# Optimization experiments

Hardware: AMD Instinct MI355X
Metric: run time of the kernel (lower is better)

The kernel has to match this reference:

```python
import jax, jax.numpy as jnp
import numpy as np

B, N, P, K = 4, 512, 1024, 20
LMAX, SH_DIM, MUL, NB = 2, 9, 64, 20
CUT, T, NSPEC = 4.0, 3, 119
E = N * K
PE = P * K
L_SLICES = [(0, 1), (1, 4), (4, 9)]


def spherical_harmonics(vec):
    # component-normalized real SH up to l=2 on the unit vector (e3nn 'component' norm: ||Y_l||^2 = 2l+1)
    r = jnp.sqrt(jnp.sum(vec * vec, axis=-1, keepdims=True))
    u = vec / jnp.maximum(r, 1e-9)
    x, y, z = u[:, 0], u[:, 1], u[:, 2]
    s3, s5, s15 = 3.0 ** 0.5, 5.0 ** 0.5, 15.0 ** 0.5
    return jnp.stack([
        jnp.ones_like(x),
        s3 * x, s3 * y, s3 * z,
        s15 * x * y, s15 * y * z, 0.5 * s5 * (3.0 * z * z - 1.0),
        s15 * x * z, 0.5 * s15 * (x * x - y * y),
    ], axis=-1)  # [E, 9]


def radial_basis(r):
    # gaussian RBF, centers linspace(0, cutoff, num_basis)
    centers = jnp.linspace(0.0, CUT, NB)
    sigma = CUT / NB
    return jnp.exp(-((r[:, None] - centers[None, :]) / sigma) ** 2)


def per_l_linear(a, Wl):
    # a: [n, 9, mul]; Wl: [3, mul, mul]; independent channel-mixing per angular momentum l
    return jnp.concatenate([a[:, s:e, :] @ Wl[l] for l, (s, e) in enumerate(L_SLICES)], axis=1)


def conv_layer(h_src_feats, sh, rbf, src, dst, n_out, Wr1, br1, Wr2, br2, Wl, Wg):
    # radial MLP -> per-edge weights; gather scalar source features; tensor-product-style message sh (x) (w*s)
    w = jax.nn.silu(rbf @ Wr1 + br1) @ Wr2 + br2                 # [E, mul]
    s_src = h_src_feats[src, 0, :]                               # [E, mul]
    m = sh[:, :, None] * (s_src * w)[:, None, :]                 # [E, 9, mul]
    a = jax.ops.segment_sum(m, dst, num_segments=n_out) / (K ** 0.5)
    u = per_l_linear(a, Wl)                                      # [n, 9, mul]
    gate = jax.nn.sigmoid(a[:, 0, :] @ Wg)                       # gate activation for l>0
    return jnp.concatenate([jax.nn.silu(u[:, :1, :]), u[:, 1:, :] * gate[:, None, :]], axis=1)


def _forward(atom_xyz, atom_edges_displacement, cell, probe_xyz, probe_edges_displacement,
             W_embed, Wr1, br1, Wr2, br2, Wl, Wg,
             pWr1, pbr1, pWr2, pbr2, pWl, pWg, W_out,
             atom_edges, probe_edges, nodes):
    Na, Np, Et, PEt = B * N, B * P, B * E, B * PE
    pos = atom_xyz.reshape(Na, 3)          # unpad_and_cat with uniform lengths == reshape
    ppos = probe_xyz.reshape(Np, 3)
    node_off = (jnp.arange(B, dtype=atom_edges.dtype) * N)[:, None, None]
    a_edges = (atom_edges + node_off).reshape(Et, 2)
    p_off = jnp.concatenate([node_off, (jnp.arange(B, dtype=atom_edges.dtype) * P)[:, None, None]], axis=2)
    p_edges = (probe_edges + p_off).reshape(PEt, 2)
    # fractional displacement -> cartesian via per-graph cell (repeat_interleave over edges)
    cell_a = jnp.repeat(cell, E, axis=0)
    cell_p = jnp.repeat(cell, PE, axis=0)
    disp_a = jnp.einsum('ei,eij->ej', atom_edges_displacement.reshape(Et, 3), cell_a)
    disp_p = jnp.einsum('ei,eij->ej', probe_edges_displacement.reshape(PEt, 3), cell_p)
    src, dst = a_edges[:, 0], a_edges[:, 1]
    edge_vec = pos[dst] - (pos[src] + disp_a)
    sh = spherical_harmonics(edge_vec)
    rbf = radial_basis(jnp.linalg.norm(edge_vec, axis=1))
    psrc, pdst = p_edges[:, 0], p_edges[:, 1]
    p_vec = ppos[pdst] - (pos[psrc] + disp_p)
    psh = spherical_harmonics(p_vec)
    prbf = radial_basis(jnp.linalg.norm(p_vec, axis=1))
    # AtomicConfigurationModel: one-hot species -> scalar channel, T interaction layers, keep per-layer reps
    onehot = jax.nn.one_hot(nodes.reshape(Na), NSPEC, dtype=W_embed.dtype)
    h = jnp.zeros((Na, SH_DIM, MUL), W_embed.dtype).at[:, 0, :].set(onehot @ W_embed)
    reps = []
    for t in range(T):
        h = h + conv_layer(h, sh, rbf, src, dst, Na, Wr1[t], br1[t], Wr2[t], br2[t], Wl[t], Wg[t])
        reps.append(h)
    # AtomicPotentialModel: atom->probe message passing using per-layer atom representations
    p = jnp.zeros((Np, SH_DIM, MUL), W_embed.dtype)
    for t in range(T):
        p = p + conv_layer(reps[t], psh, prbf, psrc, pdst, Np, pWr1[t], pbr1[t], pWr2[t], pbr2[t], pWl[t], pWg[t])
    out = (p[:, 0, :] @ W_out)[:, 0].reshape(B, P)  # readout to 0e scalar, pad_and_stack == reshape
    return out


def setup_inputs():
    key = jax.random.key(0)
    ks = jax.random.split(key, 20)
    f32 = jnp.float32
    atom_xyz = jax.random.uniform(ks[0], (B, N, 3), f32) * 8.0
    probe_xyz = jax.random.uniform(ks[1], (B, P, 3), f32) * 8.0
    cell = jnp.tile(jnp.eye(3, dtype=f32)[None] * 8.0, (B, 1, 1))
    atom_edges = jax.random.randint(ks[2], (B, E, 2), 0, N, jnp.int32)
    probe_edges = jnp.concatenate([
        jax.random.randint(ks[3], (B, PE, 1), 0, N, jnp.int32),
        jax.random.randint(ks[4], (B, PE, 1), 0, P, jnp.int32)], axis=2)
    atom_edges_displacement = jax.random.randint(ks[5], (B, E, 3), -1, 2).astype(f32)
    probe_edges_displacement = jax.random.randint(ks[6], (B, PE, 3), -1, 2).astype(f32)
    nodes = jax.random.randint(ks[7], (B, N), 1, 84, jnp.int32)
    num_nodes = jnp.full((B,), N, jnp.int32)
    num_atom_edges = jnp.full((B,), E, jnp.int32)
    num_probes = jnp.full((B,), P, jnp.int32)
    num_probe_edges = jnp.full((B,), PE, jnp.int32)
    rn = lambda k, s: jax.random.normal(k, s, f32) * 0.1
    W_embed = rn(ks[8], (NSPEC, MUL))
    Wr1 = rn(ks[9], (T, NB, 100)); br1 = jnp.zeros((T, 100), f32)
    Wr2 = rn(ks[10], (T, 100, MUL)); br2 = jnp.zeros((T, MUL), f32)
    Wl = rn(ks[11], (T, 3, MUL, MUL)); Wg = rn(ks[12], (T, MUL, MUL))
    pWr1 = rn(ks[13], (T, NB, 100)); pbr1 = jnp.zeros((T, 100), f32)
    pWr2 = rn(ks[14], (T, 100, MUL)); pbr2 = jnp.zeros((T, MUL), f32)
    pWl = rn(ks[15], (T, 3, MUL, MUL)); pWg = rn(ks[16], (T, MUL, MUL))
    W_out = rn(ks[17], (MUL, 1))
    return dict(atom_xyz=atom_xyz, atom_edges_displacement=atom_edges_displacement, cell=cell,
                probe_xyz=probe_xyz, probe_edges_displacement=probe_edges_displacement,
                W_embed=W_embed, Wr1=Wr1, br1=br1, Wr2=Wr2, br2=br2, Wl=Wl, Wg=Wg,
                pWr1=pWr1, pbr1=pbr1, pWr2=pWr2, pbr2=pbr2, pWl=pWl, pWg=pWg, W_out=W_out,
                atom_edges=atom_edges, probe_edges=probe_edges, nodes=nodes,
                num_nodes=num_nodes, num_atom_edges=num_atom_edges,
                num_probes=num_probes, num_probe_edges=num_probe_edges)


def reference(atom_xyz, atom_edges_displacement, cell, probe_xyz, probe_edges_displacement,
              W_embed, Wr1, br1, Wr2, br2, Wl, Wg,
              pWr1, pbr1, pWr2, pbr2, pWl, pWg, W_out,
              atom_edges, probe_edges, nodes, num_nodes, num_atom_edges, num_probes, num_probe_edges):
    # num_* are uniform (all graphs same size); unpad_and_cat reduces to reshape.
    return _forward(atom_xyz, atom_edges_displacement, cell, probe_xyz, probe_edges_displacement,
                    W_embed, Wr1, br1, Wr2, br2, Wl, Wg,
                    pWr1, pbr1, pWr2, pbr2, pWl, pWg, W_out,
                    atom_edges, probe_edges, nodes)
```

## Files before the change

kernel.cpp:

```cpp
#include <hip/hip_runtime.h>
#include <math.h>

#define Bc 4
#define Nc 512
#define Pc 1024
#define Kc 20
#define MUL 64
#define NBc 20
#define HID 100
#define Tc 3
#define CUTc 4.0f
#define Ec (Nc * Kc)
#define PEc (Pc * Kc)
#define NA (Bc * Nc)
#define NP (Bc * Pc)
#define ET (Bc * Ec)
#define PET (Bc * PEc)
#define TBL 2048
#define RMAXT 6.5f
#define CAP 64
#define TROWS 4
#define TBLOCKS (6 * TBL / TROWS)
#define ZBLOCKS 8
#define EBLOCKS 32

__device__ __forceinline__ float silu_f(float x) { return x / (1.0f + __expf(-x)); }
__device__ __forceinline__ float lane_bcast_f(float v, int l) {
    return __int_as_float(__builtin_amdgcn_readlane(__float_as_int(v), l));
}

__global__ __launch_bounds__(256) void front_kernel(
    const float* __restrict__ Wr1, const float* __restrict__ pWr1,
    const float* __restrict__ br1, const float* __restrict__ pbr1,
    const float* __restrict__ Wr2, const float* __restrict__ pWr2,
    const float* __restrict__ br2, const float* __restrict__ pbr2,
    const int* __restrict__ nodes, const float* __restrict__ Wemb,
    int* __restrict__ cnt_both, float* __restrict__ h0row,
    float* __restrict__ wtab)
{
    __shared__ float Hs[TROWS * HID];
    int bid = blockIdx.x;
    int t = threadIdx.x;

    if (bid < TBLOCKS) {
        int grow0 = bid * TROWS;
        int ly = grow0 / TBL;
        int t3 = (ly < 3) ? ly : ly - 3;
        const float* w1 = ((ly < 3) ? Wr1 : pWr1) + (size_t)t3 * NBc * HID;
        const float* b1 = ((ly < 3) ? br1 : pbr1) + (size_t)t3 * HID;
        const float* w2 = ((ly < 3) ? Wr2 : pWr2) + (size_t)t3 * HID * MUL;
        const float* b2 = ((ly < 3) ? br2 : pbr2) + (size_t)t3 * MUL;
        const float step = CUTc / (NBc - 1);
        const float inv_sigma = (float)NBc / CUTc;

        for (int id = t; id < TROWS * HID; id += 256) {
            int il = id / HID, j = id - il * HID;
            float r = (float)(grow0 % TBL + il) * (RMAXT / (float)TBL);
            float s = b1[j];
#pragma unroll
            for (int k = 0; k < NBc; ++k) {
                float tt = (r - k * step) * inv_sigma;
                s = fmaf(__expf(-tt * tt), w1[k * HID + j], s);
            }
            Hs[id] = silu_f(s);
        }
        __syncthreads();

        int il = t >> 6, c = t & 63;
        float acc = b2[c];
#pragma unroll 4
        for (int j = 0; j < HID; ++j)
            acc = fmaf(Hs[il * HID + j], w2[(size_t)j * MUL + c], acc);
        wtab[(size_t)(grow0 + il) * MUL + c] = acc;
    } else if (bid < TBLOCKS + ZBLOCKS) {
        int idx = (bid - TBLOCKS) * 256 + t;
        for (int i = idx; i < NA + NP; i += ZBLOCKS * 256) cnt_both[i] = 0;
    } else {
        int idx = (bid - TBLOCKS - ZBLOCKS) * 256 + t;
        for (int i = idx; i < NA * MUL; i += EBLOCKS * 256) {
            int a = i >> 6, c = i & 63;
            h0row[i] = Wemb[nodes[a] * MUL + c];
        }
    }
}

__global__ void geom_kernel(const float* __restrict__ apos,
                            const float* __restrict__ ppos,
                            const int* __restrict__ a_edges,
                            const int* __restrict__ p_edges,
                            const float* __restrict__ a_disp,
                            const float* __restrict__ p_disp,
                            const float* __restrict__ cell,
                            int* __restrict__ cnt_a, int* __restrict__ cnt_p,
                            float* __restrict__ br_a, int* __restrict__ bs_a,
                            float* __restrict__ br_p, int* __restrict__ bs_p)
{
    int e = blockIdx.x * 256 + threadIdx.x;
    if (e >= ET + PET) return;
    const int* edges; const float* displ; const float* pdst;
    int* cnt; float* brout; int* bsout;
    int el, Eper, dst_stride;
    if (e < ET) {
        el = e; edges = a_edges; displ = a_disp; pdst = apos;
        Eper = Ec; dst_stride = Nc; cnt = cnt_a; brout = br_a; bsout = bs_a;
    } else {
        el = e - ET; edges = p_edges; displ = p_disp; pdst = ppos;
        Eper = PEc; dst_stride = Pc; cnt = cnt_p; brout = br_p; bsout = bs_p;
    }
    int b = el / Eper;
    int sg = edges[el * 2 + 0] + b * Nc;
    int dg = edges[el * 2 + 1] + b * dst_stride;
    const float* C = cell + b * 9;
    float d0 = displ[el * 3 + 0], d1 = displ[el * 3 + 1], d2 = displ[el * 3 + 2];
    float dx = d0 * C[0] + d1 * C[3] + d2 * C[6];
    float dy = d0 * C[1] + d1 * C[4] + d2 * C[7];
    float dz = d0 * C[2] + d1 * C[5] + d2 * C[8];
    float vx = pdst[dg * 3 + 0] - (apos[sg * 3 + 0] + dx);
    float vy = pdst[dg * 3 + 1] - (apos[sg * 3 + 1] + dy);
    float vz = pdst[dg * 3 + 2] - (apos[sg * 3 + 2] + dz);
    float r = sqrtf(vx * vx + vy * vy + vz * vz);
    int pos = atomicAdd(&cnt[dg], 1);
    if (pos < CAP) {
        brout[(size_t)dg * CAP + pos] = r;
        bsout[(size_t)dg * CAP + pos] = sg;
    }
}

__global__ __launch_bounds__(256) void layer_kernel(
    const float* __restrict__ hsrc,
    float* __restrict__ outb,
    const int* __restrict__ cnt,
    const float* __restrict__ brk, const int* __restrict__ bsk,
    const float* __restrict__ wtab,
    const float* __restrict__ Wl0)
{
    __shared__ float tile[4][64];
    int c = threadIdx.x & 63;
    int w = threadIdx.x >> 6;
    int n = blockIdx.x * 4 + w;

    int m = min(cnt[n], CAP);
    float rvec = 0.0f; int svec = 0;
    if (c < m) { rvec = brk[(size_t)n * CAP + c]; svec = bsk[(size_t)n * CAP + c]; }
    float acc = 0.0f;
    const float scale = (float)TBL / RMAXT;
#pragma unroll 4
    for (int p = 0; p < m; ++p) {
        float rr = lane_bcast_f(rvec, p);
        int sg = __builtin_amdgcn_readlane(svec, p);
        float x = fminf(rr * scale, (float)TBL - 1.001f);
        int i0 = (int)x;
        float f = x - (float)i0;
        const float* tp = wtab + (size_t)i0 * MUL;
        float w0 = tp[c];
        float w1 = tp[MUL + c];
        float wv = fmaf(w1 - w0, f, w0);
        acc = fmaf(hsrc[(size_t)sg * MUL + c], wv, acc);
    }
    acc *= 0.22360679774997896f;

    tile[w][c] = acc;
    float u = 0.0f;
#pragma unroll
    for (int k4 = 0; k4 < 16; ++k4) {
        float4 av = *(const float4*)&tile[w][k4 * 4];
        u = fmaf(av.x, Wl0[(k4 * 4 + 0) * 64 + c], u);
        u = fmaf(av.y, Wl0[(k4 * 4 + 1) * 64 + c], u);
        u = fmaf(av.z, Wl0[(k4 * 4 + 2) * 64 + c], u);
        u = fmaf(av.w, Wl0[(k4 * 4 + 3) * 64 + c], u);
    }
    outb[(size_t)n * MUL + c] = hsrc[(size_t)n * MUL + c] + silu_f(u);
}

__global__ __launch_bounds__(256) void probe3_kernel(
    const float* __restrict__ rep0, const float* __restrict__ rep1,
    const float* __restrict__ rep2,
    const int* __restrict__ cnt,
    const float* __restrict__ brk, const int* __restrict__ bsk,
    const float* __restrict__ wtab,
    const float* __restrict__ pWl,
    const float* __restrict__ Wout,
    float* __restrict__ out)
{
    __shared__ float tile[4][64];
    int c = threadIdx.x & 63;
    int w = threadIdx.x >> 6;
    int n = blockIdx.x * 4 + w;

    int m = min(cnt[n], CAP);
    float rvec = 0.0f; int svec = 0;
    if (c < m) { rvec = brk[(size_t)n * CAP + c]; svec = bsk[(size_t)n * CAP + c]; }
    float acc0 = 0.0f, acc1 = 0.0f, acc2 = 0.0f;
    const float scale = (float)TBL / RMAXT;
    const float* wt0 = wtab;
    const float* wt1 = wtab + (size_t)TBL * MUL;
    const float* wt2 = wtab + (size_t)2 * TBL * MUL;
#pragma unroll 2
    for (int p = 0; p < m; ++p) {
        float rr = lane_bcast_f(rvec, p);
        int sg = __builtin_amdgcn_readlane(svec, p);
        float x = fminf(rr * scale, (float)TBL - 1.001f);
        int i0 = (int)x;
        float f = x - (float)i0;
        size_t rowo = (size_t)i0 * MUL + c;
        float wv0 = fmaf(wt0[rowo + MUL] - wt0[rowo], f, wt0[rowo]);
        float wv1 = fmaf(wt1[rowo + MUL] - wt1[rowo], f, wt1[rowo]);
        float wv2 = fmaf(wt2[rowo + MUL] - wt2[rowo], f, wt2[rowo]);
        size_t so = (size_t)sg * MUL + c;
        acc0 = fmaf(rep0[so], wv0, acc0);
        acc1 = fmaf(rep1[so], wv1, acc1);
        acc2 = fmaf(rep2[so], wv2, acc2);
    }
    const float isk = 0.22360679774997896f;
    float res = 0.0f;
    float accs[3] = {acc0, acc1, acc2};
#pragma unroll
    for (int t = 0; t < 3; ++t) {
        tile[w][c] = accs[t] * isk;
        const float* W = pWl + (size_t)t * 3 * MUL * MUL;
        float u = 0.0f;
#pragma unroll
        for (int k4 = 0; k4 < 16; ++k4) {
            float4 av = *(const float4*)&tile[w][k4 * 4];
            u = fmaf(av.x, W[(k4 * 4 + 0) * 64 + c], u);
            u = fmaf(av.y, W[(k4 * 4 + 1) * 64 + c], u);
            u = fmaf(av.z, W[(k4 * 4 + 2) * 64 + c], u);
            u = fmaf(av.w, W[(k4 * 4 + 3) * 64 + c], u);
        }
        res += silu_f(u);
    }

    float v = res * Wout[c];
#pragma unroll
    for (int o = 32; o > 0; o >>= 1) v += __shfl_down(v, o, 64);
    if (c == 0) out[n] = v;
}

extern "C" void kernel_launch(void* const* d_in, const int* in_sizes, int n_in,
                              void* d_out, int out_size, void* d_ws, size_t ws_size,
                              hipStream_t stream)
{
    const float* atom_xyz  = (const float*)d_in[0];
    const float* a_disp    = (const float*)d_in[1];
    const float* cell      = (const float*)d_in[2];
    const float* probe_xyz = (const float*)d_in[3];
    const float* p_disp    = (const float*)d_in[4];
    const float* W_embed   = (const float*)d_in[5];
    const float* Wr1       = (const float*)d_in[6];
    const float* br1       = (const float*)d_in[7];
    const float* Wr2       = (const float*)d_in[8];
    const float* br2       = (const float*)d_in[9];
    const float* Wl        = (const float*)d_in[10];
    const float* pWr1      = (const float*)d_in[12];
    const float* pbr1      = (const float*)d_in[13];
    const float* pWr2      = (const float*)d_in[14];
    const float* pbr2      = (const float*)d_in[15];
    const float* pWl       = (const float*)d_in[16];
    const float* W_out     = (const float*)d_in[18];
    const int*   atom_edges  = (const int*)d_in[19];
    const int*   probe_edges = (const int*)d_in[20];
    const int*   nodes       = (const int*)d_in[21];
    float* out = (float*)d_out;

    char* w = (char*)d_ws;
    auto alloc = [&](size_t bytes) -> void* {
        void* r = (void*)w;
        w += (bytes + 255) & ~(size_t)255;
        return r;
    };
    int*   cnt_both = (int*)alloc((size_t)(NA + NP) * 4);
    int*   cnt_a  = cnt_both;
    int*   cnt_p  = cnt_both + NA;
    float* br_a   = (float*)alloc((size_t)NA * CAP * 4);
    int*   bs_a   = (int*)alloc((size_t)NA * CAP * 4);
    float* br_p   = (float*)alloc((size_t)NP * CAP * 4);
    int*   bs_p   = (int*)alloc((size_t)NP * CAP * 4);
    float* h0row  = (float*)alloc((size_t)NA * MUL * 4);
    float* rep0   = (float*)alloc((size_t)NA * MUL * 4);
    float* rep1   = (float*)alloc((size_t)NA * MUL * 4);
    float* rep2   = (float*)alloc((size_t)NA * MUL * 4);
    float* wtab   = (float*)alloc((size_t)6 * TBL * MUL * 4);

    front_kernel<<<TBLOCKS + ZBLOCKS + EBLOCKS, 256, 0, stream>>>(
        Wr1, pWr1, br1, pbr1, Wr2, pWr2, br2, pbr2,
        nodes, W_embed, cnt_both, h0row, wtab);

    geom_kernel<<<(ET + PET + 255) / 256, 256, 0, stream>>>(
        atom_xyz, probe_xyz, atom_edges, probe_edges, a_disp, p_disp, cell,
        cnt_a, cnt_p, br_a, bs_a, br_p, bs_p);

    const float* hprev = h0row;
    float* reps[3] = {rep0, rep1, rep2};
    for (int t = 0; t < Tc; ++t) {
        layer_kernel<<<NA / 4, 256, 0, stream>>>(
            hprev, reps[t], cnt_a, br_a, bs_a,
            wtab + (size_t)t * TBL * MUL,
            Wl + (size_t)t * 3 * MUL * MUL);
        hprev = reps[t];
    }

    probe3_kernel<<<NP / 4, 256, 0, stream>>>(
        rep0, rep1, rep2, cnt_p, br_p, bs_p,
        wtab + (size_t)3 * TBL * MUL, pWl, W_out, out);
}
```

Measured before the change: 85.88 us.

## Store radial table as value+slope pairs and split edge loop across two waves

The radial-weight table now stores each entry as a float2 of value and slope to the next row, so each edge lookup costs one 8-byte load instead of two separate loads plus a subtraction. The front kernel computes one extra row per block so the slope can be formed. The layer and probe kernels now give each node two wavefronts, each handling alternate edges and half of the 64x64 channel mix, combining partials through shared memory. This doubles the parallelism available for latency hiding in the gather-heavy loops, at the cost of a larger table, extra barriers and launching twice as many blocks.

```diff
diff --git a/kernel.cpp b/kernel.cpp
--- a/kernel.cpp
+++ b/kernel.cpp
@@ -36,15 +36,17 @@
     const float* __restrict__ br2, const float* __restrict__ pbr2,
     const int* __restrict__ nodes, const float* __restrict__ Wemb,
     int* __restrict__ cnt_both, float* __restrict__ h0row,
-    float* __restrict__ wtab)
-{
-    __shared__ float Hs[TROWS * HID];
+    float2* __restrict__ wtab)
+{
+    __shared__ float Hs[(TROWS + 1) * HID];
+    __shared__ float Ws[(TROWS + 1) * MUL];
     int bid = blockIdx.x;
     int t = threadIdx.x;
 
     if (bid < TBLOCKS) {
         int grow0 = bid * TROWS;
         int ly = grow0 / TBL;
+        int rin = grow0 % TBL;
         int t3 = (ly < 3) ? ly : ly - 3;
         const float* w1 = ((ly < 3) ? Wr1 : pWr1) + (size_t)t3 * NBc * HID;
         const float* b1 = ((ly < 3) ? br1 : pbr1) + (size_t)t3 * HID;
@@ -53,9 +55,9 @@
         const float step = CUTc / (NBc - 1);
         const float inv_sigma = (float)NBc / CUTc;
 
-        for (int id = t; id < TROWS * HID; id += 256) {
+        for (int id = t; id < (TROWS + 1) * HID; id += 256) {
             int il = id / HID, j = id - il * HID;
-            float r = (float)(grow0 % TBL + il) * (RMAXT / (float)TBL);
+            float r = (float)(rin + il) * (RMAXT / (float)TBL);
             float s = b1[j];
 #pragma unroll
             for (int k = 0; k < NBc; ++k) {
@@ -66,12 +68,22 @@
         }
         __syncthreads();
 
-        int il = t >> 6, c = t & 63;
-        float acc = b2[c];
+        for (int id = t; id < (TROWS + 1) * MUL; id += 256) {
+            int il = id >> 6, c = id & 63;
+            float acc = b2[c];
 #pragma unroll 4
-        for (int j = 0; j < HID; ++j)
-            acc = fmaf(Hs[il * HID + j], w2[(size_t)j * MUL + c], acc);
-        wtab[(size_t)(grow0 + il) * MUL + c] = acc;
+            for (int j = 0; j < HID; ++j)
+                acc = fmaf(Hs[il * HID + j], w2[(size_t)j * MUL + c], acc);
+            Ws[id] = acc;
+        }
+        __syncthreads();
+
+        {
+            int il = t >> 6, c = t & 63;
+            float w0 = Ws[il * MUL + c];
+            float w1v = Ws[(il + 1) * MUL + c];
+            wtab[(size_t)(grow0 + il) * MUL + c] = make_float2(w0, w1v - w0);
+        }
     } else if (bid < TBLOCKS + ZBLOCKS) {
         int idx = (bid - TBLOCKS) * 256 + t;
         for (int i = idx; i < NA + NP; i += ZBLOCKS * 256) cnt_both[i] = 0;
@@ -131,13 +143,17 @@
     float* __restrict__ outb,
     const int* __restrict__ cnt,
     const float* __restrict__ brk, const int* __restrict__ bsk,
-    const float* __restrict__ wtab,
+    const float2* __restrict__ wtab,
     const float* __restrict__ Wl0)
 {
-    __shared__ float tile[4][64];
-    int c = threadIdx.x & 63;
-    int w = threadIdx.x >> 6;
-    int n = blockIdx.x * 4 + w;
+    __shared__ float tileA[2][2][64];
+    __shared__ float tileU[2][2][64];
+    int t = threadIdx.x;
+    int c = t & 63;
+    int wv = t >> 6;
+    int nb = wv >> 1;
+    int q  = wv & 1;
+    int n = blockIdx.x * 2 + nb;
 
     int m = min(cnt[n], CAP);
     float rvec = 0.0f; int svec = 0;
@@ -145,31 +161,38 @@
     float acc = 0.0f;
     const float scale = (float)TBL / RMAXT;
 #pragma unroll 4
-    for (int p = 0; p < m; ++p) {
+    for (int p = q; p < m; p += 2) {
         float rr = lane_bcast_f(rvec, p);
         int sg = __builtin_amdgcn_readlane(svec, p);
         float x = fminf(rr * scale, (float)TBL - 1.001f);
         int i0 = (int)x;
         float f = x - (float)i0;
-        const float* tp = wtab + (size_t)i0 * MUL;
-        float w0 = tp[c];
-        float w1 = tp[MUL + c];
-        float wv = fmaf(w1 - w0, f, w0);
-        acc = fmaf(hsrc[(size_t)sg * MUL + c], wv, acc);
-    }
-    acc *= 0.22360679774997896f;
-
-    tile[w][c] = acc;
+        float2 v = wtab[(size_t)i0 * MUL + c];
+        float wvv = fmaf(v.y, f, v.x);
+        acc = fmaf(hsrc[(size_t)sg * MUL + c], wvv, acc);
+    }
+    tileA[nb][q][c] = acc;
+    __syncthreads();
+
+    const float isk = 0.22360679774997896f;
     float u = 0.0f;
-#pragma unroll
-    for (int k4 = 0; k4 < 16; ++k4) {
-        float4 av = *(const float4*)&tile[w][k4 * 4];
-        u = fmaf(av.x, Wl0[(k4 * 4 + 0) * 64 + c], u);
-        u = fmaf(av.y, Wl0[(k4 * 4 + 1) * 64 + c], u);
-        u = fmaf(av.z, Wl0[(k4 * 4 + 2) * 64 + c], u);
-        u = fmaf(av.w, Wl0[(k4 * 4 + 3) * 64 + c], u);
-    }
-    outb[(size_t)n * MUL + c] = hsrc[(size_t)n * MUL + c] + silu_f(u);
+    int k0 = q * 32;
+#pragma unroll
+    for (int k4 = 0; k4 < 8; ++k4) {
+        int k = k0 + k4 * 4;
+        float4 a0 = *(const float4*)&tileA[nb][0][k];
+        float4 a1 = *(const float4*)&tileA[nb][1][k];
+        u = fmaf((a0.x + a1.x) * isk, Wl0[(k + 0) * 64 + c], u);
+        u = fmaf((a0.y + a1.y) * isk, Wl0[(k + 1) * 64 + c], u);
+        u = fmaf((a0.z + a1.z) * isk, Wl0[(k + 2) * 64 + c], u);
+        u = fmaf((a0.w + a1.w) * isk, Wl0[(k + 3) * 64 + c], u);
+    }
+    tileU[nb][q][c] = u;
+    __syncthreads();
+    if (q == 0) {
+        float uu = tileU[nb][0][c] + tileU[nb][1][c];
+        outb[(size_t)n * MUL + c] = hsrc[(size_t)n * MUL + c] + silu_f(uu);
+    }
 }
 
 __global__ __launch_bounds__(256) void probe3_kernel(
@@ -177,63 +200,80 @@
     const float* __restrict__ rep2,
     const int* __restrict__ cnt,
     const float* __restrict__ brk, const int* __restrict__ bsk,
-    const float* __restrict__ wtab,
+    const float2* __restrict__ wtab,
     const float* __restrict__ pWl,
     const float* __restrict__ Wout,
     float* __restrict__ out)
 {
-    __shared__ float tile[4][64];
-    int c = threadIdx.x & 63;
-    int w = threadIdx.x >> 6;
-    int n = blockIdx.x * 4 + w;
+    __shared__ float tileA[2][2][3][64];
+    __shared__ float tileU[2][2][3][64];
+    int t = threadIdx.x;
+    int c = t & 63;
+    int wv = t >> 6;
+    int nb = wv >> 1;
+    int q  = wv & 1;
+    int n = blockIdx.x * 2 + nb;
 
     int m = min(cnt[n], CAP);
     float rvec = 0.0f; int svec = 0;
     if (c < m) { rvec = brk[(size_t)n * CAP + c]; svec = bsk[(size_t)n * CAP + c]; }
     float acc0 = 0.0f, acc1 = 0.0f, acc2 = 0.0f;
     const float scale = (float)TBL / RMAXT;
-    const float* wt0 = wtab;
-    const float* wt1 = wtab + (size_t)TBL * MUL;
-    const float* wt2 = wtab + (size_t)2 * TBL * MUL;
+    const float2* wt0 = wtab;
+    const float2* wt1 = wtab + (size_t)TBL * MUL;
+    const float2* wt2 = wtab + (size_t)2 * TBL * MUL;
 #pragma unroll 2
-    for (int p = 0; p < m; ++p) {
+    for (int p = q; p < m; p += 2) {
         float rr = lane_bcast_f(rvec, p);
         int sg = __builtin_amdgcn_readlane(svec, p);
         float x = fminf(rr * scale, (float)TBL - 1.001f);
         int i0 = (int)x;
         float f = x - (float)i0;
         size_t rowo = (size_t)i0 * MUL + c;
-        float wv0 = fmaf(wt0[rowo + MUL] - wt0[rowo], f, wt0[rowo]);
-        float wv1 = fmaf(wt1[rowo + MUL] - wt1[rowo], f, wt1[rowo]);
-        float wv2 = fmaf(wt2[rowo + MUL] - wt2[rowo], f, wt2[rowo]);
+        float2 v0 = wt0[rowo], v1 = wt1[rowo], v2 = wt2[rowo];
+        float wv0 = fmaf(v0.y, f, v0.x);
+        float wv1 = fmaf(v1.y, f, v1.x);
+        float wv2 = fmaf(v2.y, f, v2.x);
         size_t so = (size_t)sg * MUL + c;
         acc0 = fmaf(rep0[so], wv0, acc0);
         acc1 = fmaf(rep1[so], wv1, acc1);
         acc2 = fmaf(rep2[so], wv2, acc2);
     }
+    tileA[nb][q][0][c] = acc0;
+    tileA[nb][q][1][c] = acc1;
+    tileA[nb][q][2][c] = acc2;
+    __syncthreads();
+
     const float isk = 0.22360679774997896f;
-    float res = 0.0f;
-    float accs[3] = {acc0, acc1, acc2};
-#pragma unroll
-    for (int t = 0; t < 3; ++t) {
-        tile[w][c] = accs[t] * isk;
-        const float* W = pWl + (size_t)t * 3 * MUL * MUL;
+    int k0 = q * 32;
+#pragma unroll
+    for (int tt = 0; tt < 3; ++tt) {
+        const float* W = pWl + (size_t)tt * 3 * MUL * MUL;
         float u = 0.0f;
 #pragma unroll
-        for (int k4 = 0; k4 < 16; ++k4) {
-            float4 av = *(const float4*)&tile[w][k4 * 4];
-            u = fmaf(av.x, W[(k4 * 4 + 0) * 64 + c], u);
-            u = fmaf(av.y, W[(k4 * 4 + 1) * 64 + c], u);
-            u = fmaf(av.z, W[(k4 * 4 + 2) * 64 + c], u);
-            u = fmaf(av.w, W[(k4 * 4 + 3) * 64 + c], u);
-        }
-        res += silu_f(u);
-    }
-
-    float v = res * Wout[c];
-#pragma unroll
-    for (int o = 32; o > 0; o >>= 1) v += __shfl_down(v, o, 64);
-    if (c == 0) out[n] = v;
+        for (int k4 = 0; k4 < 8; ++k4) {
+            int k = k0 + k4 * 4;
+            float4 a0 = *(const float4*)&tileA[nb][0][tt][k];
+            float4 a1 = *(const float4*)&tileA[nb][1][tt][k];
+            u = fmaf((a0.x + a1.x) * isk, W[(k + 0) * 64 + c], u);
+            u = fmaf((a0.y + a1.y) * isk, W[(k + 1) * 64 + c], u);
+            u = fmaf((a0.z + a1.z) * isk, W[(k + 2) * 64 + c], u);
+            u = fmaf((a0.w + a1.w) * isk, W[(k + 3) * 64 + c], u);
+        }
+        tileU[nb][q][tt][c] = u;
+    }
+    __syncthreads();
+
+    if (q == 0) {
+        float res = 0.0f;
+#pragma unroll
+        for (int tt = 0; tt < 3; ++tt)
+            res += silu_f(tileU[nb][0][tt][c] + tileU[nb][1][tt][c]);
+        float v = res * Wout[c];
+#pragma unroll
+        for (int o = 32; o > 0; o >>= 1) v += __shfl_down(v, o, 64);
+        if (c == 0) out[n] = v;
+    }
 }
 
 extern "C" void kernel_launch(void* const* d_in, const int* in_sizes, int n_in,
@@ -279,7 +319,7 @@
     float* rep0   = (float*)alloc((size_t)NA * MUL * 4);
     float* rep1   = (float*)alloc((size_t)NA * MUL * 4);
     float* rep2   = (float*)alloc((size_t)NA * MUL * 4);
-    float* wtab   = (float*)alloc((size_t)6 * TBL * MUL * 4);
+    float2* wtab  = (float2*)alloc((size_t)6 * TBL * MUL * 8);
 
     front_kernel<<<TBLOCKS + ZBLOCKS + EBLOCKS, 256, 0, stream>>>(
         Wr1, pWr1, br1, pbr1, Wr2, pWr2, br2, pbr2,
@@ -292,14 +332,14 @@
     const float* hprev = h0row;
     float* reps[3] = {rep0, rep1, rep2};
     for (int t = 0; t < Tc; ++t) {
-        layer_kernel<<<NA / 4, 256, 0, stream>>>(
+        layer_kernel<<<NA / 2, 256, 0, stream>>>(
             hprev, reps[t], cnt_a, br_a, bs_a,
             wtab + (size_t)t * TBL * MUL,
             Wl + (size_t)t * 3 * MUL * MUL);
         hprev = reps[t];
     }
 
-    probe3_kernel<<<NP / 4, 256, 0, stream>>>(
+    probe3_kernel<<<NP / 2, 256, 0, stream>>>(
         rep0, rep1, rep2, cnt_p, br_p, bs_p,
         wtab + (size_t)3 * TBL * MUL, pWl, W_out, out);
 }
```

Result: slower. 88.91 us (+3.5%).

## Store radial tables as value/delta pairs and interleave layer outputs

Applied to the files above, without the earlier changes.

The radial-weight tables now store (w0, w1-w0) pairs, so each interpolation takes one vector load instead of two scalar loads. The probe tables for the three layers are packed into float4+float2 per entry. The three layer representations are interleaved into one float4-strided buffer, so the probe kernel gathers all three source features with a single float4 load. The table is also shrunk to 1024 rows over a smaller radius range; this cuts front-kernel work but coarsens the interpolation and risks clamping edges whose distance exceeds 5.25. Layer kernels now read and write with strides of 4, which makes those accesses uncoalesced.

```diff
diff --git a/kernel.cpp b/kernel.cpp
--- a/kernel.cpp
+++ b/kernel.cpp
@@ -16,8 +16,8 @@
 #define NP (Bc * Pc)
 #define ET (Bc * Ec)
 #define PET (Bc * PEc)
-#define TBL 2048
-#define RMAXT 6.5f
+#define TBL 1024
+#define RMAXT 5.25f
 #define CAP 64
 #define TROWS 4
 #define TBLOCKS (6 * TBL / TROWS)
@@ -36,15 +36,19 @@
     const float* __restrict__ br2, const float* __restrict__ pbr2,
     const int* __restrict__ nodes, const float* __restrict__ Wemb,
     int* __restrict__ cnt_both, float* __restrict__ h0row,
-    float* __restrict__ wtab)
-{
-    __shared__ float Hs[TROWS * HID];
+    float2* __restrict__ awtab,
+    float2* __restrict__ pw4,
+    float2* __restrict__ pw2)
+{
+    __shared__ float Hs[(TROWS + 1) * HID];
+    __shared__ float Ws[(TROWS + 1) * MUL];
     int bid = blockIdx.x;
     int t = threadIdx.x;
 
     if (bid < TBLOCKS) {
         int grow0 = bid * TROWS;
         int ly = grow0 / TBL;
+        int rin = grow0 % TBL;
         int t3 = (ly < 3) ? ly : ly - 3;
         const float* w1 = ((ly < 3) ? Wr1 : pWr1) + (size_t)t3 * NBc * HID;
         const float* b1 = ((ly < 3) ? br1 : pbr1) + (size_t)t3 * HID;
@@ -53,9 +57,9 @@
         const float step = CUTc / (NBc - 1);
         const float inv_sigma = (float)NBc / CUTc;
 
-        for (int id = t; id < TROWS * HID; id += 256) {
+        for (int id = t; id < (TROWS + 1) * HID; id += 256) {
             int il = id / HID, j = id - il * HID;
-            float r = (float)(grow0 % TBL + il) * (RMAXT / (float)TBL);
+            float r = (float)(rin + il) * (RMAXT / (float)TBL);
             float s = b1[j];
 #pragma unroll
             for (int k = 0; k < NBc; ++k) {
@@ -66,12 +70,29 @@
         }
         __syncthreads();
 
-        int il = t >> 6, c = t & 63;
-        float acc = b2[c];
+        for (int id = t; id < (TROWS + 1) * MUL; id += 256) {
+            int il = id >> 6, c = id & 63;
+            float acc = b2[c];
 #pragma unroll 4
-        for (int j = 0; j < HID; ++j)
-            acc = fmaf(Hs[il * HID + j], w2[(size_t)j * MUL + c], acc);
-        wtab[(size_t)(grow0 + il) * MUL + c] = acc;
+            for (int j = 0; j < HID; ++j)
+                acc = fmaf(Hs[il * HID + j], w2[(size_t)j * MUL + c], acc);
+            Ws[id] = acc;
+        }
+        __syncthreads();
+
+        {
+            int il = t >> 6, c = t & 63;
+            int row = rin + il;
+            float w0 = Ws[il * MUL + c];
+            float dw = Ws[(il + 1) * MUL + c] - w0;
+            if (ly < 3) {
+                awtab[((size_t)ly * TBL + row) * MUL + c] = make_float2(w0, dw);
+            } else if (t3 < 2) {
+                pw4[((size_t)row * MUL + c) * 2 + t3] = make_float2(w0, dw);
+            } else {
+                pw2[(size_t)row * MUL + c] = make_float2(w0, dw);
+            }
+        }
     } else if (bid < TBLOCKS + ZBLOCKS) {
         int idx = (bid - TBLOCKS) * 256 + t;
         for (int i = idx; i < NA + NP; i += ZBLOCKS * 256) cnt_both[i] = 0;
@@ -127,11 +148,12 @@
 }
 
 __global__ __launch_bounds__(256) void layer_kernel(
-    const float* __restrict__ hsrc,
-    float* __restrict__ outb,
+    const float* __restrict__ hread,
+    int hs,
+    float* __restrict__ wrt,
     const int* __restrict__ cnt,
     const float* __restrict__ brk, const int* __restrict__ bsk,
-    const float* __restrict__ wtab,
+    const float2* __restrict__ wtab,
     const float* __restrict__ Wl0)
 {
     __shared__ float tile[4][64];
@@ -151,11 +173,9 @@
         float x = fminf(rr * scale, (float)TBL - 1.001f);
         int i0 = (int)x;
         float f = x - (float)i0;
-        const float* tp = wtab + (size_t)i0 * MUL;
-        float w0 = tp[c];
-        float w1 = tp[MUL + c];
-        float wv = fmaf(w1 - w0, f, w0);
-        acc = fmaf(hsrc[(size_t)sg * MUL + c], wv, acc);
+        float2 v = wtab[(size_t)i0 * MUL + c];
+        float wvv = fmaf(v.y, f, v.x);
+        acc = fmaf(hread[((size_t)sg * MUL + c) * hs], wvv, acc);
     }
     acc *= 0.22360679774997896f;
 
@@ -169,15 +189,16 @@
         u = fmaf(av.z, Wl0[(k4 * 4 + 2) * 64 + c], u);
         u = fmaf(av.w, Wl0[(k4 * 4 + 3) * 64 + c], u);
     }
-    outb[(size_t)n * MUL + c] = hsrc[(size_t)n * MUL + c] + silu_f(u);
+    size_t idx = (size_t)n * MUL + c;
+    wrt[idx * 4] = hread[idx * hs] + silu_f(u);
 }
 
 __global__ __launch_bounds__(256) void probe3_kernel(
-    const float* __restrict__ rep0, const float* __restrict__ rep1,
-    const float* __restrict__ rep2,
+    const float4* __restrict__ rep4,
     const int* __restrict__ cnt,
     const float* __restrict__ brk, const int* __restrict__ bsk,
-    const float* __restrict__ wtab,
+    const float4* __restrict__ pw4,
+    const float2* __restrict__ pw2,
     const float* __restrict__ pWl,
     const float* __restrict__ Wout,
     float* __restrict__ out)
@@ -192,9 +213,6 @@
     if (c < m) { rvec = brk[(size_t)n * CAP + c]; svec = bsk[(size_t)n * CAP + c]; }
     float acc0 = 0.0f, acc1 = 0.0f, acc2 = 0.0f;
     const float scale = (float)TBL / RMAXT;
-    const float* wt0 = wtab;
-    const float* wt1 = wtab + (size_t)TBL * MUL;
-    const float* wt2 = wtab + (size_t)2 * TBL * MUL;
 #pragma unroll 2
     for (int p = 0; p < m; ++p) {
         float rr = lane_bcast_f(rvec, p);
@@ -203,21 +221,23 @@
         int i0 = (int)x;
         float f = x - (float)i0;
         size_t rowo = (size_t)i0 * MUL + c;
-        float wv0 = fmaf(wt0[rowo + MUL] - wt0[rowo], f, wt0[rowo]);
-        float wv1 = fmaf(wt1[rowo + MUL] - wt1[rowo], f, wt1[rowo]);
-        float wv2 = fmaf(wt2[rowo + MUL] - wt2[rowo], f, wt2[rowo]);
-        size_t so = (size_t)sg * MUL + c;
-        acc0 = fmaf(rep0[so], wv0, acc0);
-        acc1 = fmaf(rep1[so], wv1, acc1);
-        acc2 = fmaf(rep2[so], wv2, acc2);
+        float4 v01 = pw4[rowo];
+        float2 v2  = pw2[rowo];
+        float wv0 = fmaf(v01.y, f, v01.x);
+        float wv1 = fmaf(v01.w, f, v01.z);
+        float wv2 = fmaf(v2.y,  f, v2.x);
+        float4 rv = rep4[(size_t)sg * MUL + c];
+        acc0 = fmaf(rv.x, wv0, acc0);
+        acc1 = fmaf(rv.y, wv1, acc1);
+        acc2 = fmaf(rv.z, wv2, acc2);
     }
     const float isk = 0.22360679774997896f;
     float res = 0.0f;
     float accs[3] = {acc0, acc1, acc2};
 #pragma unroll
-    for (int t = 0; t < 3; ++t) {
-        tile[w][c] = accs[t] * isk;
-        const float* W = pWl + (size_t)t * 3 * MUL * MUL;
+    for (int tt = 0; tt < 3; ++tt) {
+        tile[w][c] = accs[tt] * isk;
+        const float* W = pWl + (size_t)tt * 3 * MUL * MUL;
         float u = 0.0f;
 #pragma unroll
         for (int k4 = 0; k4 < 16; ++k4) {
@@ -276,30 +296,29 @@
     float* br_p   = (float*)alloc((size_t)NP * CAP * 4);
     int*   bs_p   = (int*)alloc((size_t)NP * CAP * 4);
     float* h0row  = (float*)alloc((size_t)NA * MUL * 4);
-    float* rep0   = (float*)alloc((size_t)NA * MUL * 4);
-    float* rep1   = (float*)alloc((size_t)NA * MUL * 4);
-    float* rep2   = (float*)alloc((size_t)NA * MUL * 4);
-    float* wtab   = (float*)alloc((size_t)6 * TBL * MUL * 4);
+    float* rep4   = (float*)alloc((size_t)NA * MUL * 16);
+    float2* awtab = (float2*)alloc((size_t)3 * TBL * MUL * 8);
+    float2* pw4   = (float2*)alloc((size_t)TBL * MUL * 16);
+    float2* pw2   = (float2*)alloc((size_t)TBL * MUL * 8);
 
     front_kernel<<<TBLOCKS + ZBLOCKS + EBLOCKS, 256, 0, stream>>>(
         Wr1, pWr1, br1, pbr1, Wr2, pWr2, br2, pbr2,
-        nodes, W_embed, cnt_both, h0row, wtab);
+        nodes, W_embed, cnt_both, h0row, awtab, pw4, pw2);
 
     geom_kernel<<<(ET + PET + 255) / 256, 256, 0, stream>>>(
         atom_xyz, probe_xyz, atom_edges, probe_edges, a_disp, p_disp, cell,
         cnt_a, cnt_p, br_a, bs_a, br_p, bs_p);
 
-    const float* hprev = h0row;
-    float* reps[3] = {rep0, rep1, rep2};
     for (int t = 0; t < Tc; ++t) {
+        const float* hread = (t == 0) ? h0row : (rep4 + (t - 1));
+        int hs = (t == 0) ? 1 : 4;
         layer_kernel<<<NA / 4, 256, 0, stream>>>(
-            hprev, reps[t], cnt_a, br_a, bs_a,
-            wtab + (size_t)t * TBL * MUL,
+            hread, hs, rep4 + t, cnt_a, br_a, bs_a,
+            awtab + (size_t)t * TBL * MUL,
             Wl + (size_t)t * 3 * MUL * MUL);
-        hprev = reps[t];
     }
 
     probe3_kernel<<<NP / 4, 256, 0, stream>>>(
-        rep0, rep1, rep2, cnt_p, br_p, bs_p,
-        wtab + (size_t)3 * TBL * MUL, pWl, W_out, out);
-}
+        (const float4*)rep4, cnt_p, br_p, bs_p,
+        (const float4*)pw4, pw2, pWl, W_out, out);
+}
```

After: 87.47 us. Within noise of the previous version (+1.8%).
